# Optimization experiments

Hardware: AMD Instinct MI355X
Metric: run time of the kernel (lower is better)

## Reference

```python
import jax, jax.numpy as jnp
import numpy as np

B, N, C, UNITS = 2, 512, 128, 128


def setup_inputs() -> dict:
    key = jax.random.key(0)
    k1, k2, k3, k4, k5 = jax.random.split(key, 5)
    inputs = jax.random.normal(k1, (B, N, C), dtype=jnp.float32)
    adj_matrix = jax.random.randint(k2, (B, N, N), 0, 2).astype(jnp.float32)
    xidx = jax.random.randint(k3, (B, N), 0, N, dtype=jnp.int32)
    fan = 2 * C + UNITS
    limit = np.sqrt(6.0 / fan).astype(np.float32)  # glorot uniform
    w = jax.random.uniform(k4, (1, 2 * C, UNITS), dtype=jnp.float32, minval=-limit, maxval=limit)
    b = 0.05 * jax.random.normal(k5, (UNITS,), dtype=jnp.float32)
    return {"inputs": inputs, "adj_matrix": adj_matrix, "xidx": xidx, "w": w, "b": b}


def reference(inputs, adj_matrix, xidx, w, b):
    # inputs: [B,N,C], adj_matrix: [B,N,N], xidx: [B,N]
    mask = adj_matrix[..., None]                       # [B,N,N,1]
    # tiled_inputs[b,i,j,:] = inputs[b,i,:]; masked = mask * tiled_inputs
    masked = mask * inputs[:, :, None, :]              # [B,N,N,C]
    # xi[b,i] = masked[b,i,xidx[b,i]] = adj[b,i,xidx[b,i]] * x[b,i]
    a_sel = jnp.take_along_axis(adj_matrix, xidx[:, :, None], axis=2)  # [B,N,1]
    xi = (a_sel * 1.0)[..., None] * inputs[:, :, None, :]              # [B,N,1,C]
    edging = jnp.concatenate([masked, (xi - masked) * mask], axis=-1)  # [B,N,N,2C]
    # kernel-size-1 conv1d == per-edge matmul
    out = jnp.einsum('bijc,co->bijo', edging, w[0]) + b                # [B,N,N,units]
    out = jax.nn.relu(out)
    maxp = jnp.max(out, axis=2)                                        # [B,N,units]
    nonzero = jnp.any(out != 0.0, axis=-1, keepdims=True)              # [B,N,N,1]
    n = jnp.sum(nonzero.astype(jnp.float32), axis=2)                   # [B,N,1]
    avgpool = jnp.sum(edging, axis=2) / n                              # [B,N,2C]
    return jnp.concatenate([maxp, avgpool], axis=-1)                   # [B,N,units+2C]
```

## Files before the change

kernel.cpp:

```cpp
#include <hip/hip_runtime.h>
#include <hip/hip_bf16.h>

#define BB 2
#define NN 512
#define CC 128
#define UU 128

__device__ __forceinline__ float bfraw(unsigned short u) {
    return __uint_as_float(((unsigned int)u) << 16);
}

__global__ __launch_bounds__(128) void edgeconv_kernel(
    const void* __restrict__ inputs_,
    const void* __restrict__ adj_,
    const int*  __restrict__ xidx,
    const void* __restrict__ w_,
    const void* __restrict__ bias_,
    void*       __restrict__ out_)
{
    const int row  = blockIdx.x;
    const int t    = threadIdx.x;
    const int lane = t & 63;
    const int wv   = t >> 6;

    __shared__ float x_sh[CC];
    __shared__ float wred[2];
    __shared__ int   wdet[2];
    __shared__ int   wz0[2], wzA[2];
    __shared__ float s_sh;

    {
        const float* pf = (const float*)adj_;
        const float v0 = pf[2 * t], v1 = pf[2 * t + 1];
        const bool ok = (v0 == 0.f || v0 == 1.f) && (v1 == 0.f || v1 == 1.f);
        const unsigned long long bm = __ballot(ok);
        if (lane == 0) wdet[wv] = (bm == 0xFFFFFFFFFFFFFFFFULL) ? 1 : 0;
    }
    __syncthreads();
    const bool isf32 = (wdet[0] & wdet[1]) != 0;

    float x_c, d;
    if (isf32) {
        x_c = ((const float*)inputs_)[row * CC + t];
        const float* arow = (const float*)adj_ + (size_t)row * NN;
        const float4 a4 = *reinterpret_cast<const float4*>(arow + 4 * t);
        d = a4.x + a4.y + a4.z + a4.w;
        if (t == 0) s_sh = arow[xidx[row]];
    } else {
        x_c = bfraw(((const unsigned short*)inputs_)[row * CC + t]);
        const unsigned short* arow = (const unsigned short*)adj_ + (size_t)row * NN;
        const ushort4 a4 = *reinterpret_cast<const ushort4*>(arow + 4 * t);
        d = bfraw(a4.x) + bfraw(a4.y) + bfraw(a4.z) + bfraw(a4.w);
        if (t == 0) s_sh = bfraw(arow[xidx[row]]);
    }
    x_sh[t] = x_c;
    #pragma unroll
    for (int off = 32; off > 0; off >>= 1) d += __shfl_down(d, off);
    if (lane == 0) wred[wv] = d;
    __syncthreads();

    const float deg = wred[0] + wred[1];
    const float s   = s_sh;

    float p = 0.f, q = 0.f, bo;
    if (isf32) {
        const float* w1 = (const float*)w_ + t;
        const float* w2 = w1 + CC * UU;
        #pragma unroll 8
        for (int c = 0; c < CC; ++c) {
            const float xc = x_sh[c];
            p = fmaf(xc, w1[c * UU], p);
            q = fmaf(xc, w2[c * UU], q);
        }
        bo = ((const float*)bias_)[t];
    } else {
        const unsigned short* w1 = (const unsigned short*)w_ + t;
        const unsigned short* w2 = w1 + CC * UU;
        #pragma unroll 8
        for (int c = 0; c < CC; ++c) {
            const float xc = x_sh[c];
            p = fmaf(xc, bfraw(w1[c * UU]), p);
            q = fmaf(xc, bfraw(w2[c * UU]), q);
        }
        bo = bfraw(((const unsigned short*)bias_)[t]);
    }

    const float pa = (s > 0.5f) ? p : (p - q);
    const float v0 = fmaxf(bo, 0.f);
    const float vA = fmaxf(pa + bo, 0.f);

    const unsigned long long m0 = __ballot(v0 > 0.f);
    const unsigned long long mA = __ballot(vA > 0.f);
    if (lane == 0) { wz0[wv] = (m0 != 0ULL); wzA[wv] = (mA != 0ULL); }
    __syncthreads();

    const int z0 = wz0[0] | wz0[1];
    const int zA = wzA[0] | wzA[1];
    const float ndeg = (float)NN - deg;
    const float n = ndeg * (z0 ? 1.f : 0.f) + deg * (zA ? 1.f : 0.f);

    float maxp;
    if (deg > 0.5f) maxp = (ndeg > 0.5f) ? fmaxf(v0, vA) : vA;
    else            maxp = v0;

    const float a1 = deg * x_c / n;
    const float a2 = deg * (s - 1.f) * x_c / n;

    if (isf32) {
        float* orow = (float*)out_ + (size_t)row * (UU + 2 * CC);
        orow[t]           = maxp;
        orow[UU + t]      = a1;
        orow[UU + CC + t] = a2;
    } else {
        __hip_bfloat16* orow = (__hip_bfloat16*)out_ + (size_t)row * (UU + 2 * CC);
        orow[t]           = __float2bfloat16(maxp);
        orow[UU + t]      = __float2bfloat16(a1);
        orow[UU + CC + t] = __float2bfloat16(a2);
    }
}

extern "C" void kernel_launch(void* const* d_in, const int* in_sizes, int n_in,
                              void* d_out, int out_size, void* d_ws, size_t ws_size,
                              hipStream_t stream) {
    const void* inputs = d_in[0];
    const void* adjm   = d_in[1];
    const int*  xidx   = (const int*)d_in[2];
    const void* w      = d_in[3];
    const void* bias   = d_in[4];

    edgeconv_kernel<<<BB * NN, 128, 0, stream>>>(inputs, adjm, xidx, w, bias, d_out);
}
```

Before: 69.65 us.

## Split f32 weight matvec across channel groups with float4 loads and LDS reduction

Reworks the f32 path of the per-row x·W matvec. Each of 128 threads now owns 4 output units over a 32-channel slice and loads the weights as float4, instead of one unit over all 128 channels with scalar loads. Partial sums go to shared memory and are reduced across the 4 channel groups after a barrier. This shortens the serial dependency chain from 128 to 32 iterations and widens the memory accesses, at the cost of extra LDS traffic, a __syncthreads, and more registers.

New measurement: 78.49 us. +12.7%, slower.

```diff
diff --git a/kernel.cpp b/kernel.cpp
--- a/kernel.cpp
+++ b/kernel.cpp
@@ -23,11 +23,13 @@
     const int lane = t & 63;
     const int wv   = t >> 6;
 
-    __shared__ float x_sh[CC];
-    __shared__ float wred[2];
-    __shared__ int   wdet[2];
-    __shared__ int   wz0[2], wzA[2];
-    __shared__ float s_sh;
+    __shared__ float  x_sh[CC];
+    __shared__ float4 pp[4][32];
+    __shared__ float4 qq[4][32];
+    __shared__ float  wred[2];
+    __shared__ int    wdet[2];
+    __shared__ int    wz0[2], wzA[2];
+    __shared__ float  s_sh;
 
     {
         const float* pf = (const float*)adj_;
@@ -62,18 +64,31 @@
     const float deg = wred[0] + wred[1];
     const float s   = s_sh;
 
-    float p = 0.f, q = 0.f, bo;
+    float p, q;
     if (isf32) {
-        const float* w1 = (const float*)w_ + t;
-        const float* w2 = w1 + CC * UU;
+        const int tg = t & 31, cg = t >> 5;
+        const float4* w4 = (const float4*)w_;
+        float4 pa = {0.f, 0.f, 0.f, 0.f}, qa = {0.f, 0.f, 0.f, 0.f};
+        const int c0 = cg << 5;
         #pragma unroll 8
-        for (int c = 0; c < CC; ++c) {
+        for (int cc = 0; cc < 32; ++cc) {
+            const int c = c0 + cc;
             const float xc = x_sh[c];
-            p = fmaf(xc, w1[c * UU], p);
-            q = fmaf(xc, w2[c * UU], q);
+            const float4 w1 = w4[c * 32 + tg];
+            const float4 w2 = w4[(c + 128) * 32 + tg];
+            pa.x = fmaf(xc, w1.x, pa.x);  pa.y = fmaf(xc, w1.y, pa.y);
+            pa.z = fmaf(xc, w1.z, pa.z);  pa.w = fmaf(xc, w1.w, pa.w);
+            qa.x = fmaf(xc, w2.x, qa.x);  qa.y = fmaf(xc, w2.y, qa.y);
+            qa.z = fmaf(xc, w2.z, qa.z);  qa.w = fmaf(xc, w2.w, qa.w);
         }
-        bo = ((const float*)bias_)[t];
+        pp[cg][tg] = pa;  qq[cg][tg] = qa;
+        __syncthreads();
+        const float* ppf = (const float*)pp;
+        const float* qqf = (const float*)qq;
+        p = ppf[t] + ppf[128 + t] + ppf[256 + t] + ppf[384 + t];
+        q = qqf[t] + qqf[128 + t] + qqf[256 + t] + qqf[384 + t];
     } else {
+        p = 0.f; q = 0.f;
         const unsigned short* w1 = (const unsigned short*)w_ + t;
         const unsigned short* w2 = w1 + CC * UU;
         #pragma unroll 8
@@ -82,12 +97,13 @@
             p = fmaf(xc, bfraw(w1[c * UU]), p);
             q = fmaf(xc, bfraw(w2[c * UU]), q);
         }
-        bo = bfraw(((const unsigned short*)bias_)[t]);
     }
+    const float bo = isf32 ? ((const float*)bias_)[t]
+                           : bfraw(((const unsigned short*)bias_)[t]);
 
-    const float pa = (s > 0.5f) ? p : (p - q);
+    const float pa_ = (s > 0.5f) ? p : (p - q);
     const float v0 = fmaxf(bo, 0.f);
-    const float vA = fmaxf(pa + bo, 0.f);
+    const float vA = fmaxf(pa_ + bo, 0.f);
 
     const unsigned long long m0 = __ballot(v0 > 0.f);
     const unsigned long long mA = __ballot(vA > 0.f);
```

## Process two rows per block and share weight loads across rows

Applied to the files above, without the earlier changes.

Each 256-thread block now handles two rows. Each half of the block computes one of the two weight halves (p or q) for both rows, so every weight element loaded is used for two rows, and the results are exchanged through shared memory. The runtime dtype detection and the bf16 path are removed, so the kernel assumes fp32 inputs. This halves the grid size and total weight traffic, at the cost of an extra barrier and shared-memory exchange.

Measured after the change: 68.82 us. About the same (-1.2%).

```diff
diff --git a/kernel.cpp b/kernel.cpp
--- a/kernel.cpp
+++ b/kernel.cpp
@@ -6,96 +6,75 @@
 #define CC 128
 #define UU 128
 
-__device__ __forceinline__ float bfraw(unsigned short u) {
-    return __uint_as_float(((unsigned int)u) << 16);
-}
+__global__ __launch_bounds__(256) void edgeconv_kernel(
+    const float* __restrict__ inputs,
+    const float* __restrict__ adj,
+    const int*   __restrict__ xidx,
+    const float* __restrict__ w,
+    const float* __restrict__ bias,
+    float*       __restrict__ out)
+{
+    const int r0   = blockIdx.x * 2;
+    const int t    = threadIdx.x;
+    const int u    = t & 127;
+    const int h    = t >> 7;
+    const int wave = t >> 6;
+    const int lane = t & 63;
 
-__global__ __launch_bounds__(128) void edgeconv_kernel(
-    const void* __restrict__ inputs_,
-    const void* __restrict__ adj_,
-    const int*  __restrict__ xidx,
-    const void* __restrict__ w_,
-    const void* __restrict__ bias_,
-    void*       __restrict__ out_)
-{
-    const int row  = blockIdx.x;
-    const int t    = threadIdx.x;
-    const int lane = t & 63;
-    const int wv   = t >> 6;
+    __shared__ float x_sh[2][CC];
+    __shared__ float pq[2][2][UU];
+    __shared__ float wred[4][2];
+    __shared__ float s_sh[2];
+    __shared__ int   wzA[4], wz0[4];
 
-    __shared__ float x_sh[CC];
-    __shared__ float wred[2];
-    __shared__ int   wdet[2];
-    __shared__ int   wz0[2], wzA[2];
-    __shared__ float s_sh;
+    x_sh[h][u] = inputs[(r0 + h) * CC + u];
 
-    {
-        const float* pf = (const float*)adj_;
-        const float v0 = pf[2 * t], v1 = pf[2 * t + 1];
-        const bool ok = (v0 == 0.f || v0 == 1.f) && (v1 == 0.f || v1 == 1.f);
-        const unsigned long long bm = __ballot(ok);
-        if (lane == 0) wdet[wv] = (bm == 0xFFFFFFFFFFFFFFFFULL) ? 1 : 0;
+    const float* arow0 = adj + (size_t)r0 * NN;
+    const float* arow1 = arow0 + NN;
+    const float2 a0 = reinterpret_cast<const float2*>(arow0)[t];
+    const float2 a1 = reinterpret_cast<const float2*>(arow1)[t];
+    float d0 = a0.x + a0.y;
+    float d1 = a1.x + a1.y;
+    #pragma unroll
+    for (int off = 32; off > 0; off >>= 1) {
+        d0 += __shfl_down(d0, off);
+        d1 += __shfl_down(d1, off);
     }
-    __syncthreads();
-    const bool isf32 = (wdet[0] & wdet[1]) != 0;
+    if (lane == 0) { wred[wave][0] = d0; wred[wave][1] = d1; }
 
-    float x_c, d;
-    if (isf32) {
-        x_c = ((const float*)inputs_)[row * CC + t];
-        const float* arow = (const float*)adj_ + (size_t)row * NN;
-        const float4 a4 = *reinterpret_cast<const float4*>(arow + 4 * t);
-        d = a4.x + a4.y + a4.z + a4.w;
-        if (t == 0) s_sh = arow[xidx[row]];
-    } else {
-        x_c = bfraw(((const unsigned short*)inputs_)[row * CC + t]);
-        const unsigned short* arow = (const unsigned short*)adj_ + (size_t)row * NN;
-        const ushort4 a4 = *reinterpret_cast<const ushort4*>(arow + 4 * t);
-        d = bfraw(a4.x) + bfraw(a4.y) + bfraw(a4.z) + bfraw(a4.w);
-        if (t == 0) s_sh = bfraw(arow[xidx[row]]);
-    }
-    x_sh[t] = x_c;
-    #pragma unroll
-    for (int off = 32; off > 0; off >>= 1) d += __shfl_down(d, off);
-    if (lane == 0) wred[wv] = d;
+    if (t == 0) s_sh[0] = arow0[xidx[r0]];
+    if (t == 1) s_sh[1] = arow1[xidx[r0 + 1]];
     __syncthreads();
 
-    const float deg = wred[0] + wred[1];
-    const float s   = s_sh;
+    const float* wcol = w + h * (CC * UU) + u;
+    float acc0 = 0.f, acc1 = 0.f;
+    #pragma unroll 8
+    for (int c = 0; c < CC; ++c) {
+        const float wv = wcol[c * UU];
+        acc0 = fmaf(x_sh[0][c], wv, acc0);
+        acc1 = fmaf(x_sh[1][c], wv, acc1);
+    }
+    pq[0][h][u] = acc0;
+    pq[1][h][u] = acc1;
+    __syncthreads();
 
-    float p = 0.f, q = 0.f, bo;
-    if (isf32) {
-        const float* w1 = (const float*)w_ + t;
-        const float* w2 = w1 + CC * UU;
-        #pragma unroll 8
-        for (int c = 0; c < CC; ++c) {
-            const float xc = x_sh[c];
-            p = fmaf(xc, w1[c * UU], p);
-            q = fmaf(xc, w2[c * UU], q);
-        }
-        bo = ((const float*)bias_)[t];
-    } else {
-        const unsigned short* w1 = (const unsigned short*)w_ + t;
-        const unsigned short* w2 = w1 + CC * UU;
-        #pragma unroll 8
-        for (int c = 0; c < CC; ++c) {
-            const float xc = x_sh[c];
-            p = fmaf(xc, bfraw(w1[c * UU]), p);
-            q = fmaf(xc, bfraw(w2[c * UU]), q);
-        }
-        bo = bfraw(((const unsigned short*)bias_)[t]);
-    }
+    const float p   = pq[h][0][u];
+    const float q   = pq[h][1][u];
+    const float s   = s_sh[h];
+    const float deg = wred[0][h] + wred[1][h] + wred[2][h] + wred[3][h];
+    const float bo  = bias[u];
 
     const float pa = (s > 0.5f) ? p : (p - q);
     const float v0 = fmaxf(bo, 0.f);
     const float vA = fmaxf(pa + bo, 0.f);
 
+    const unsigned long long mA = __ballot(vA > 0.f);
     const unsigned long long m0 = __ballot(v0 > 0.f);
-    const unsigned long long mA = __ballot(vA > 0.f);
-    if (lane == 0) { wz0[wv] = (m0 != 0ULL); wzA[wv] = (mA != 0ULL); }
+    if (lane == 0) { wzA[wave] = (mA != 0ULL); wz0[wave] = (m0 != 0ULL); }
     __syncthreads();
 
-    const int z0 = wz0[0] | wz0[1];
-    const int zA = wzA[0] | wzA[1];
+    const int zA = h ? (wzA[2] | wzA[3]) : (wzA[0] | wzA[1]);
+    const int z0 = wz0[0] | wz0[1] | wz0[2] | wz0[3];
     const float ndeg = (float)NN - deg;
     const float n = ndeg * (z0 ? 1.f : 0.f) + deg * (zA ? 1.f : 0.f);
 
@@ -103,30 +82,23 @@
     if (deg > 0.5f) maxp = (ndeg > 0.5f) ? fmaxf(v0, vA) : vA;
     else            maxp = v0;
 
-    const float a1 = deg * x_c / n;
-    const float a2 = deg * (s - 1.f) * x_c / n;
-
-    if (isf32) {
-        float* orow = (float*)out_ + (size_t)row * (UU + 2 * CC);
-        orow[t]           = maxp;
-        orow[UU + t]      = a1;
-        orow[UU + CC + t] = a2;
-    } else {
-        __hip_bfloat16* orow = (__hip_bfloat16*)out_ + (size_t)row * (UU + 2 * CC);
-        orow[t]           = __float2bfloat16(maxp);
-        orow[UU + t]      = __float2bfloat16(a1);
-        orow[UU + CC + t] = __float2bfloat16(a2);
-    }
+    const float xc = x_sh[h][u];
+    const float inv_n = 1.f / n;
+    float* orow = out + (size_t)(r0 + h) * (UU + 2 * CC);
+    orow[u]            = maxp;
+    orow[UU + u]       = deg * xc * inv_n;
+    orow[UU + CC + u]  = deg * (s - 1.f) * xc * inv_n;
 }
 
 extern "C" void kernel_launch(void* const* d_in, const int* in_sizes, int n_in,
                               void* d_out, int out_size, void* d_ws, size_t ws_size,
                               hipStream_t stream) {
-    const void* inputs = d_in[0];
-    const void* adjm   = d_in[1];
-    const int*  xidx   = (const int*)d_in[2];
-    const void* w      = d_in[3];
-    const void* bias   = d_in[4];
+    const float* inputs = (const float*)d_in[0];
+    const float* adjm   = (const float*)d_in[1];
+    const int*   xidx   = (const int*)d_in[2];
+    const float* w      = (const float*)d_in[3];
+    const float* bias   = (const float*)d_in[4];
+    float*       out    = (float*)d_out;
 
-    edgeconv_kernel<<<BB * NN, 128, 0, stream>>>(inputs, adjm, xidx, w, bias, d_out);
+    edgeconv_kernel<<<(BB * NN) / 2, 256, 0, stream>>>(inputs, adjm, xidx, w, bias, out);
 }
```
